# Performance work log

Measured on AMD Instinct MI355X. Metric: run time of the kernel, lower is better.

The kernel has to match this reference:

```python
import jax, jax.numpy as jnp
import numpy as np

B, S, H = 1, 2048, 1024
NH, KVH, HD = 16, 4, 64
E, TOPK, F = 8, 2, 2048
EPS = 1e-5
THETA = 10000.0


def setup_inputs() -> dict:
    key = jax.random.key(0)
    ks = jax.random.split(key, 12)
    s = 0.02
    return {
        "hidden_states": jax.random.normal(ks[0], (B, S, H), jnp.float32),
        "position_ids": jnp.arange(S, dtype=jnp.int64).reshape(1, S),
        "ln1_w": jnp.ones((H,), jnp.float32),
        "ln2_w": jnp.ones((H,), jnp.float32),
        "wq": jax.random.normal(ks[1], (NH * HD, H), jnp.float32) * s,
        "wk": jax.random.normal(ks[2], (KVH * HD, H), jnp.float32) * s,
        "wv": jax.random.normal(ks[3], (KVH * HD, H), jnp.float32) * s,
        "wo": jax.random.normal(ks[4], (H, NH * HD), jnp.float32) * s,
        "gate_w": jax.random.normal(ks[5], (E, H), jnp.float32) * s,
        "w1": jax.random.normal(ks[6], (E, F, H), jnp.float32) * s,
        "w2": jax.random.normal(ks[7], (E, H, F), jnp.float32) * s,
        "w3": jax.random.normal(ks[8], (E, F, H), jnp.float32) * s,
    }


def rmsnorm(x, w, eps=EPS):
    xf = x.astype(jnp.float32)
    v = jnp.mean(xf * xf, axis=-1, keepdims=True)
    return (xf * jax.lax.rsqrt(v + eps)).astype(x.dtype) * w


def rotate_half(x):
    x1, x2 = jnp.split(x, 2, axis=-1)
    return jnp.concatenate([-x2, x1], axis=-1)


def attention(x, position_ids, wq, wk, wv, wo):
    q = (x @ wq.T).reshape(B, S, NH, HD).transpose(0, 2, 1, 3)   # [B,NH,S,HD]
    k = (x @ wk.T).reshape(B, S, KVH, HD).transpose(0, 2, 1, 3)  # [B,KVH,S,HD]
    v = (x @ wv.T).reshape(B, S, KVH, HD).transpose(0, 2, 1, 3)
    inv_freq = 1.0 / (THETA ** (jnp.arange(0, HD, 2, dtype=jnp.float32) / HD))
    ang = position_ids.astype(jnp.float32)[:, :, None] * inv_freq  # [B,S,HD/2]
    emb = jnp.concatenate([ang, ang], axis=-1)                     # [B,S,HD]
    cos = jnp.cos(emb)[:, None]                                    # [B,1,S,HD]
    sin = jnp.sin(emb)[:, None]
    q = q * cos + rotate_half(q) * sin
    k = k * cos + rotate_half(k) * sin
    rep = NH // KVH
    k = jnp.repeat(k, rep, axis=1)
    v = jnp.repeat(v, rep, axis=1)
    scores = jnp.einsum("bhqd,bhkd->bhqk", q, k) / np.sqrt(HD).astype(np.float32)
    causal = jnp.tril(jnp.ones((S, S), bool))
    scores = jnp.where(causal, scores, jnp.finfo(scores.dtype).min)
    attn = jax.nn.softmax(scores, axis=-1)
    ctx = jnp.einsum("bhqk,bhkd->bhqd", attn, v)
    ctx = ctx.transpose(0, 2, 1, 3).reshape(B, S, NH * HD)
    return ctx @ wo.T


def moe(x, gate_w, w1, w2, w3):
    xt = x.reshape(-1, H)                                  # [T,H]
    router_logits = xt @ gate_w.T                          # [T,E]
    probs = jax.nn.softmax(router_logits.astype(jnp.float32), axis=-1)
    topw, topi = jax.lax.top_k(probs, TOPK)                # [T,K]
    topw = topw / jnp.sum(topw, axis=-1, keepdims=True)
    topw = topw.astype(x.dtype)
    # combine weights per expert: [T,E]
    cw = jnp.sum(topw[..., None] * jax.nn.one_hot(topi, E, dtype=x.dtype), axis=1)
    h1 = jnp.einsum("th,efh->etf", xt, w1)
    h3 = jnp.einsum("th,efh->etf", xt, w3)
    g = jax.nn.silu(h1) * h3                               # [E,T,F]
    y = jnp.einsum("etf,ehf->eth", g, w2)                  # [E,T,H]
    out = jnp.einsum("eth,te->th", y, cw)
    return out.reshape(B, S, H), router_logits


def reference(hidden_states, position_ids, ln1_w, ln2_w, wq, wk, wv, wo,
              gate_w, w1, w2, w3):
    residual = hidden_states
    h = rmsnorm(hidden_states, ln1_w)
    h = attention(h, position_ids, wq, wk, wv, wo)
    h = residual + h
    residual = h
    h = rmsnorm(h, ln2_w)
    h, router_logits = moe(h, gate_w, w1, w2, w3)
    h = residual + h
    return h, router_logits
```

## Files before the change

### kernel.cpp

```cpp
#include <hip/hip_runtime.h>
#include <hip/hip_bf16.h>
#include <cstdint>

typedef unsigned short u16;
typedef __attribute__((ext_vector_type(8))) short bh8;
typedef __attribute__((ext_vector_type(4))) short sh4;
typedef __attribute__((ext_vector_type(4))) float fx4;

#define NTOK 2048
#define HDIM 1024
#define NE 8
#define FDIM 2048

#define VMCNT(n) asm volatile("s_waitcnt vmcnt(" #n ")" ::: "memory")
#define LGKM0()  asm volatile("s_waitcnt lgkmcnt(0)" ::: "memory")
#define SBAR()   __builtin_amdgcn_s_barrier()
#define SCB()    __builtin_amdgcn_sched_barrier(0)

__device__ __forceinline__ u16 f2bf(float f) {
    __hip_bfloat16 h = __float2bfloat16(f);
    return __builtin_bit_cast(u16, h);
}

__device__ __forceinline__ void gll16(const void* g, void* l) {
    __builtin_amdgcn_global_load_lds(
        (const __attribute__((address_space(1))) void*)g,
        (__attribute__((address_space(3))) void*)l, 16, 0, 0);
}

#define N8_WQ 131072
#define N8_WK 32768
#define N8_WV 32768
#define N8_WO 131072
#define N8_W  2097152
#define B0q 0
#define B1k (B0q + N8_WQ)
#define B2v (B1k + N8_WK)
#define B3o (B2v + N8_WV)
#define B4a (B3o + N8_WO)
#define B5b (B4a + N8_W)
#define B6c (B5b + N8_W)
#define N8TOT (B6c + N8_W)

__global__ __launch_bounds__(256)
void convert_all_k(const float* __restrict__ wq, const float* __restrict__ wk,
                   const float* __restrict__ wv, const float* __restrict__ wo,
                   const float* __restrict__ w1, const float* __restrict__ w2,
                   const float* __restrict__ w3, u16* __restrict__ arena) {
    int i = blockIdx.x * 256 + threadIdx.x;
    const int stride = gridDim.x * 256;
    for (; i < N8TOT; i += stride) {
        const float* src;
        int base;
        if (i < B1k)      { src = wq; base = B0q; }
        else if (i < B2v) { src = wk; base = B1k; }
        else if (i < B3o) { src = wv; base = B2v; }
        else if (i < B4a) { src = wo; base = B3o; }
        else if (i < B5b) { src = w1; base = B4a; }
        else if (i < B6c) { src = w2; base = B5b; }
        else              { src = w3; base = B6c; }
        const size_t li = (size_t)(i - base) * 8;
        const fx4 a = *(const fx4*)&src[li];
        const fx4 b = *(const fx4*)&src[li + 4];
        bh8 o;
        #pragma unroll
        for (int j = 0; j < 4; ++j) {
            o[j]     = (short)f2bf(a[j]);
            o[j + 4] = (short)f2bf(b[j]);
        }
        *(bh8*)&arena[(size_t)i * 8] = o;
    }
}

__global__ __launch_bounds__(256)
void rope_table_k(float* __restrict__ cosT, float* __restrict__ sinT) {
    int idx = blockIdx.x * 256 + threadIdx.x;
    int t = idx >> 5, i = idx & 31;
    float freq = powf(10000.0f, -(float)i * (1.0f / 32.0f));
    float ang = (float)t * freq;
    float s, c;
    sincosf(ang, &s, &c);
    cosT[idx] = c;
    sinT[idx] = s;
}

__global__ __launch_bounds__(256)
void rmsnorm_k(const float* __restrict__ X, const float* __restrict__ W, u16* __restrict__ O) {
    const int t = blockIdx.x;
    const int tid = threadIdx.x;
    const fx4 v = *(const fx4*)&X[(size_t)t * HDIM + tid * 4];
    float ss = v[0]*v[0] + v[1]*v[1] + v[2]*v[2] + v[3]*v[3];
    #pragma unroll
    for (int o = 1; o < 64; o <<= 1) ss += __shfl_xor(ss, o);
    __shared__ float red[4];
    if ((tid & 63) == 0) red[tid >> 6] = ss;
    __syncthreads();
    const float inv = rsqrtf((red[0] + red[1] + red[2] + red[3]) * (1.0f / HDIM) + 1e-5f);
    const fx4 w = *(const fx4*)&W[tid * 4];
    sh4 o4;
    #pragma unroll
    for (int i = 0; i < 4; ++i) o4[i] = (short)f2bf(v[i] * inv * w[i]);
    *(sh4*)&O[(size_t)t * HDIM + tid * 4] = o4;
}

__global__ __launch_bounds__(256)
void rmsnorm2_router_k(const float* __restrict__ X, const float* __restrict__ W,
                       const float* __restrict__ GW, u16* __restrict__ O,
                       float* __restrict__ LOGI) {
    const int t = blockIdx.x;
    const int tid = threadIdx.x;
    const fx4 v = *(const fx4*)&X[(size_t)t * HDIM + tid * 4];
    float ss = v[0]*v[0] + v[1]*v[1] + v[2]*v[2] + v[3]*v[3];
    #pragma unroll
    for (int o = 1; o < 64; o <<= 1) ss += __shfl_xor(ss, o);
    __shared__ float red[4];
    if ((tid & 63) == 0) red[tid >> 6] = ss;
    __syncthreads();
    const float inv = rsqrtf((red[0] + red[1] + red[2] + red[3]) * (1.0f / HDIM) + 1e-5f);
    const fx4 w = *(const fx4*)&W[tid * 4];
    fx4 xn;
    #pragma unroll
    for (int i = 0; i < 4; ++i) xn[i] = v[i] * inv * w[i];
    sh4 o4;
    #pragma unroll
    for (int i = 0; i < 4; ++i) o4[i] = (short)f2bf(xn[i]);
    *(sh4*)&O[(size_t)t * HDIM + tid * 4] = o4;

    float part[NE];
    #pragma unroll
    for (int e = 0; e < NE; ++e) {
        const fx4 g = *(const fx4*)&GW[(size_t)e * HDIM + tid * 4];
        part[e] = g[0]*xn[0] + g[1]*xn[1] + g[2]*xn[2] + g[3]*xn[3];
    }
    #pragma unroll
    for (int e = 0; e < NE; ++e)
        #pragma unroll
        for (int o = 1; o < 64; o <<= 1) part[e] += __shfl_xor(part[e], o);
    __shared__ float red8[4][NE];
    if ((tid & 63) == 0) {
        #pragma unroll
        for (int e = 0; e < NE; ++e) red8[tid >> 6][e] = part[e];
    }
    __syncthreads();
    if (tid < NE)
        LOGI[(size_t)t * NE + tid] = red8[0][tid] + red8[1][tid] + red8[2][tid] + red8[3][tid];
}

__global__ __launch_bounds__(256)
void router_topk_k(const float* __restrict__ LOGI, int* __restrict__ counts,
                   int* __restrict__ tokslot, float* __restrict__ wtb) {
    const int t = blockIdx.x * 256 + threadIdx.x;
    float l[NE];
    #pragma unroll
    for (int e = 0; e < NE; ++e) l[e] = LOGI[(size_t)t * NE + e];
    int i0 = 0;
    #pragma unroll
    for (int e = 1; e < NE; ++e) if (l[e] > l[i0]) i0 = e;
    int i1 = (i0 == 0) ? 1 : 0;
    #pragma unroll
    for (int e = 0; e < NE; ++e) if (e != i0 && l[e] > l[i1]) i1 = e;
    float e1 = __expf(l[i1] - l[i0]);
    float w0 = 1.0f / (1.0f + e1);
    float w1 = 1.0f - w0;
    int p0 = atomicAdd(&counts[i0], 1);
    tokslot[i0 * NTOK + p0] = t * 2;
    wtb[i0 * NTOK + p0] = w0;
    int p1 = atomicAdd(&counts[i1], 1);
    tokslot[i1 * NTOK + p1] = t * 2 + 1;
    wtb[i1 * NTOK + p1] = w1;
}

template<int EPI>
__global__ __launch_bounds__(256)
void gemm_bt(const u16* __restrict__ A, const u16* __restrict__ B,
             u16* __restrict__ Cb, float* __restrict__ Cf,
             const int N, const int K,
             const float* __restrict__ aux0, const float* __restrict__ aux1) {
    __shared__ u16 As[2][64 * 32];
    __shared__ u16 Bs[2][64 * 32];

    const int tid = threadIdx.x;
    const int lane = tid & 63;
    const int wid = tid >> 6;
    const int lrow = lane & 15, lgrp = lane >> 4;
    const int wm = wid * 16;
    const int soff = (lgrp ^ ((lrow >> 1) & 3)) * 8;

    const int m0 = blockIdx.y * 64;
    const int n0 = blockIdx.x * 64;

    const int gseg = ((tid & 3) ^ ((tid >> 3) & 3)) * 8;
    const u16* apg = A + (size_t)(m0 + (tid >> 2)) * K + gseg;
    const u16* bpg = B + (size_t)(n0 + (tid >> 2)) * K + gseg;

    fx4 acc[4];
    #pragma unroll
    for (int i = 0; i < 4; ++i) acc[i] = fx4{0.f, 0.f, 0.f, 0.f};

    gll16(apg, &As[0][wid * 512]);
    gll16(bpg, &Bs[0][wid * 512]);

    for (int k0 = 0; k0 < K; k0 += 64) {
        gll16(apg + k0 + 32, &As[1][wid * 512]);
        gll16(bpg + k0 + 32, &Bs[1][wid * 512]);
        VMCNT(2); SBAR(); SCB();
        {
            const bh8 af = *(const bh8*)&As[0][(wm + lrow) * 32 + soff];
            #pragma unroll
            for (int ni = 0; ni < 4; ++ni) {
                const bh8 bf = *(const bh8*)&Bs[0][(ni * 16 + lrow) * 32 + soff];
                acc[ni] = __builtin_amdgcn_mfma_f32_16x16x32_bf16(af, bf, acc[ni], 0, 0, 0);
            }
        }
        LGKM0(); SBAR();
        {
            const int kn = (k0 + 64 < K) ? k0 + 64 : k0;
            gll16(apg + kn, &As[0][wid * 512]);
            gll16(bpg + kn, &Bs[0][wid * 512]);
        }
        VMCNT(2); SBAR(); SCB();
        {
            const bh8 af = *(const bh8*)&As[1][(wm + lrow) * 32 + soff];
            #pragma unroll
            for (int ni = 0; ni < 4; ++ni) {
                const bh8 bf = *(const bh8*)&Bs[1][(ni * 16 + lrow) * 32 + soff];
                acc[ni] = __builtin_amdgcn_mfma_f32_16x16x32_bf16(af, bf, acc[ni], 0, 0, 0);
            }
        }
        LGKM0(); SBAR();
    }
    VMCNT(0);

    #pragma unroll
    for (int j = 0; j < 4; ++j) {
        const int r = m0 + wm + lgrp * 4 + j;
        if (EPI == 3) {
            #pragma unroll
            for (int ni = 0; ni < 2; ++ni) {
                const int d = ni * 16 + lrow;
                const float cv = aux0[r * 32 + d];
                const float sv = aux1[r * 32 + d];
                const float v0 = acc[ni][j];
                const float v1 = acc[ni + 2][j];
                Cb[(size_t)r * N + n0 + d]      = f2bf(v0 * cv - v1 * sv);
                Cb[(size_t)r * N + n0 + d + 32] = f2bf(v1 * cv + v0 * sv);
            }
        } else {
            #pragma unroll
            for (int ni = 0; ni < 4; ++ni) {
                const int c = n0 + ni * 16 + lrow;
                const float v = acc[ni][j];
                if (EPI == 1) Cf[(size_t)r * N + c] = v + aux0[(size_t)r * N + c];
                if (EPI == 2) Cb[(size_t)r * N + c] = f2bf(v);
            }
        }
    }
}

__global__ __launch_bounds__(256)
void transpose_v_k(const u16* __restrict__ V, u16* __restrict__ VT) {
    __shared__ u16 Ls[64 * 66];
    const int tid = threadIdx.x;
    const int c0 = blockIdx.x * 64;
    const int t0 = blockIdx.y * 64;

    const int r = tid >> 2;
    const int seg = (tid & 3) * 16;
    const size_t src = (size_t)(t0 + r) * 256 + c0 + seg;
    *(bh8*)&Ls[r * 66 + seg]     = *(const bh8*)&V[src];
    *(bh8*)&Ls[r * 66 + seg + 8] = *(const bh8*)&V[src + 8];
    __syncthreads();
    const int c = tid >> 2;
    bh8 o0, o1;
    #pragma unroll
    for (int j = 0; j < 8; ++j) {
        o0[j] = (short)Ls[(seg + j) * 66 + c];
        o1[j] = (short)Ls[(seg + 8 + j) * 66 + c];
    }
    const size_t dst = (size_t)(c0 + c) * NTOK + t0 + seg;
    *(bh8*)&VT[dst]     = o0;
    *(bh8*)&VT[dst + 8] = o1;
}

__global__ __launch_bounds__(256)
void attn_part_k(const u16* __restrict__ Q, const u16* __restrict__ Kg,
                 const u16* __restrict__ VTg, float* __restrict__ pacc,
                 float* __restrict__ pl) {
    const int qt = blockIdx.x;
    const int h = blockIdx.y;
    const int c = blockIdx.z;
    if (c * 8 > qt) return;
    const int t0 = c * 8;
    const int tend = min(qt + 1, t0 + 8);
    const int kvh = h >> 2;

    const int tid = threadIdx.x;
    const int lane = tid & 63;
    const int wid = tid >> 6;
    const int lrow = lane & 15, lgrp = lane >> 4;

    __shared__ u16 Ks[64 * 66];
    __shared__ u16 Vs[64 * 66];
    __shared__ u16 Ps[4][16 * 66];

    const int qbase = qt * 64 + wid * 16;

    bh8 qf[2];
    #pragma unroll
    for (int kf = 0; kf < 2; ++kf)
        qf[kf] = *(const bh8*)&Q[(size_t)(qbase + lrow) * 1024 + h * 64 + kf * 32 + lgrp * 8];

    fx4 acc[4];
    #pragma unroll
    for (int ni = 0; ni < 4; ++ni) acc[ni] = fx4{0.f, 0.f, 0.f, 0.f};
    float lsum[4];
    #pragma unroll
    for (int j = 0; j < 4; ++j) lsum[j] = 0.f;

    const int srow = tid >> 2;
    const int sseg = (tid & 3) * 16;

    size_t gk = (size_t)(t0 * 64 + srow) * 256 + kvh * 64 + sseg;
    size_t gv = (size_t)(kvh * 64 + srow) * NTOK + t0 * 64 + sseg;
    bh8 kva = *(const bh8*)&Kg[gk];
    bh8 kvb = *(const bh8*)&Kg[gk + 8];
    bh8 vva = *(const bh8*)&VTg[gv];
    bh8 vvb = *(const bh8*)&VTg[gv + 8];

    for (int it = t0; it < tend; ++it) {
        const int kv0 = it * 64;
        __syncthreads();
        *(bh8*)&Ks[srow * 66 + sseg]     = kva;
        *(bh8*)&Ks[srow * 66 + sseg + 8] = kvb;
        *(bh8*)&Vs[srow * 66 + sseg]     = vva;
        *(bh8*)&Vs[srow * 66 + sseg + 8] = vvb;
        __syncthreads();

        const int itn = (it + 1 < tend) ? it + 1 : it;
        const size_t gk2 = (size_t)(itn * 64 + srow) * 256 + kvh * 64 + sseg;
        const size_t gv2 = (size_t)(kvh * 64 + srow) * NTOK + itn * 64 + sseg;
        kva = *(const bh8*)&Kg[gk2];
        kvb = *(const bh8*)&Kg[gk2 + 8];
        vva = *(const bh8*)&VTg[gv2];
        vvb = *(const bh8*)&VTg[gv2 + 8];

        fx4 s[4];
        #pragma unroll
        for (int nf = 0; nf < 4; ++nf) s[nf] = fx4{0.f, 0.f, 0.f, 0.f};
        #pragma unroll
        for (int kf = 0; kf < 2; ++kf) {
            #pragma unroll
            for (int nf = 0; nf < 4; ++nf) {
                const bh8 kfr = *(const bh8*)&Ks[(nf * 16 + lrow) * 66 + kf * 32 + lgrp * 8];
                s[nf] = __builtin_amdgcn_mfma_f32_16x16x32_bf16(qf[kf], kfr, s[nf], 0, 0, 0);
            }
        }

        #pragma unroll
        for (int nf = 0; nf < 4; ++nf)
            #pragma unroll
            for (int j = 0; j < 4; ++j) {
                const int qr = qbase + lgrp * 4 + j;
                const int kp = kv0 + nf * 16 + lrow;
                float p = __expf(fmaf(s[nf][j], 0.125f, -24.0f));
                p = (kp > qr) ? 0.f : p;
                s[nf][j] = p;
                lsum[j] += p;
            }

        u16* pw = Ps[wid];
        #pragma unroll
        for (int nf = 0; nf < 4; ++nf)
            #pragma unroll
            for (int j = 0; j < 4; ++j)
                pw[(lgrp * 4 + j) * 66 + nf * 16 + lrow] = f2bf(s[nf][j]);

        #pragma unroll
        for (int kf = 0; kf < 2; ++kf) {
            const bh8 pa = *(const bh8*)&pw[lrow * 66 + kf * 32 + lgrp * 8];
            #pragma unroll
            for (int ni = 0; ni < 4; ++ni) {
                const bh8 vb = *(const bh8*)&Vs[(ni * 16 + lrow) * 66 + kf * 32 + lgrp * 8];
                acc[ni] = __builtin_amdgcn_mfma_f32_16x16x32_bf16(pa, vb, acc[ni], 0, 0, 0);
            }
        }
    }

    #pragma unroll
    for (int j = 0; j < 4; ++j) {
        float l = lsum[j];
        #pragma unroll
        for (int o = 1; o < 16; o <<= 1) l += __shfl_xor(l, o);
        lsum[j] = l;
    }

    #pragma unroll
    for (int j = 0; j < 4; ++j) {
        const int r = qbase + lgrp * 4 + j;
        const size_t base = ((size_t)(h * NTOK + r) * 4 + c) * 64;
        #pragma unroll
        for (int ni = 0; ni < 4; ++ni)
            pacc[base + ni * 16 + lrow] = acc[ni][j];
        if (lrow == 0)
            pl[(size_t)(h * NTOK + r) * 4 + c] = lsum[j];
    }
}

__global__ __launch_bounds__(256)
void attn_combine_k(const float* __restrict__ pacc, const float* __restrict__ pl,
                    u16* __restrict__ O) {
    const int idx = blockIdx.x * 4 + (threadIdx.x >> 6);
    const int d = threadIdx.x & 63;
    const int h = idx >> 11;
    const int qrow = idx & 2047;
    const int nch = (qrow >> 9) + 1;

    float den = 0.f, num = 0.f;
    for (int c = 0; c < nch; ++c) {
        den += pl[(size_t)idx * 4 + c];
        num += pacc[((size_t)idx * 4 + c) * 64 + d];
    }
    O[(size_t)qrow * 1024 + h * 64 + d] = f2bf(num / den);
}

__global__ __launch_bounds__(256)
void moe_up_k(const u16* __restrict__ X, const u16* __restrict__ W1b,
              const u16* __restrict__ W3b, const int* __restrict__ counts,
              const int* __restrict__ tokslot, u16* __restrict__ G) {
    const int e = blockIdx.z;
    const int cnt = counts[e];
    const int m0 = blockIdx.y * 64;
    if (m0 >= cnt) return;
    const int n0 = blockIdx.x * 128;

    __shared__ u16 As[2][64 * 32];
    __shared__ u16 B1s[2][128 * 32];
    __shared__ u16 B3s[2][128 * 32];

    const int tid = threadIdx.x;
    const int lane = tid & 63, wid = tid >> 6;
    const int wm = (wid >> 1) * 32, wn = (wid & 1) * 64;
    const int lrow = lane & 15, lgrp = lane >> 4;
    const int soff = (lgrp ^ ((lrow >> 1) & 3)) * 8;

    const int gseg = ((tid & 3) ^ ((tid >> 3) & 3)) * 8;
    const int arow = m0 + (tid >> 2);
    const int tok = (arow < cnt) ? (tokslot[e * NTOK + arow] >> 1) : 0;
    const u16* apg = X + (size_t)tok * HDIM + gseg;
    const size_t eoff = (size_t)e * FDIM * HDIM;
    const u16* b1pg = W1b + eoff + (size_t)(n0 + (tid >> 2)) * HDIM + gseg;
    const u16* b3pg = W3b + eoff + (size_t)(n0 + (tid >> 2)) * HDIM + gseg;
    const size_t rr = (size_t)64 * HDIM;

    fx4 acc1[2][4], acc3[2][4];
    #pragma unroll
    for (int i = 0; i < 2; ++i)
        #pragma unroll
        for (int j = 0; j < 4; ++j) {
            acc1[i][j] = fx4{0.f, 0.f, 0.f, 0.f};
            acc3[i][j] = fx4{0.f, 0.f, 0.f, 0.f};
        }

    gll16(apg, &As[0][wid * 512]);
    gll16(b1pg, &B1s[0][wid * 512]);
    gll16(b1pg + rr, &B1s[0][2048 + wid * 512]);
    gll16(b3pg, &B3s[0][wid * 512]);
    gll16(b3pg + rr, &B3s[0][2048 + wid * 512]);

#define MOE_UP_COMPUTE(BUF)                                                          \
    {                                                                                \
        bh8 af[2], b1f[4], b3f[4];                                                   \
        _Pragma("unroll")                                                            \
        for (int mi = 0; mi < 2; ++mi)                                               \
            af[mi] = *(const bh8*)&As[BUF][(wm + mi * 16 + lrow) * 32 + soff];       \
        _Pragma("unroll")                                                            \
        for (int ni = 0; ni < 4; ++ni) {                                             \
            b1f[ni] = *(const bh8*)&B1s[BUF][(wn + ni * 16 + lrow) * 32 + soff];     \
            b3f[ni] = *(const bh8*)&B3s[BUF][(wn + ni * 16 + lrow) * 32 + soff];     \
        }                                                                            \
        _Pragma("unroll")                                                            \
        for (int mi = 0; mi < 2; ++mi)                                               \
            _Pragma("unroll")                                                        \
            for (int ni = 0; ni < 4; ++ni) {                                         \
                acc1[mi][ni] = __builtin_amdgcn_mfma_f32_16x16x32_bf16(af[mi], b1f[ni], acc1[mi][ni], 0, 0, 0); \
                acc3[mi][ni] = __builtin_amdgcn_mfma_f32_16x16x32_bf16(af[mi], b3f[ni], acc3[mi][ni], 0, 0, 0); \
            }                                                                        \
    }

    for (int k0 = 0; k0 < HDIM; k0 += 64) {
        {
            const int kn = k0 + 32;
            gll16(apg + kn, &As[1][wid * 512]);
            gll16(b1pg + kn, &B1s[1][wid * 512]);
            gll16(b1pg + rr + kn, &B1s[1][2048 + wid * 512]);
            gll16(b3pg + kn, &B3s[1][wid * 512]);
            gll16(b3pg + rr + kn, &B3s[1][2048 + wid * 512]);
        }
        VMCNT(5); SBAR(); SCB();
        MOE_UP_COMPUTE(0)
        LGKM0(); SBAR();
        {
            const int kn = (k0 + 64 < HDIM) ? k0 + 64 : k0;
            gll16(apg + kn, &As[0][wid * 512]);
            gll16(b1pg + kn, &B1s[0][wid * 512]);
            gll16(b1pg + rr + kn, &B1s[0][2048 + wid * 512]);
            gll16(b3pg + kn, &B3s[0][wid * 512]);
            gll16(b3pg + rr + kn, &B3s[0][2048 + wid * 512]);
        }
        VMCNT(5); SBAR(); SCB();
        MOE_UP_COMPUTE(1)
        LGKM0(); SBAR();
    }
    VMCNT(0);
#undef MOE_UP_COMPUTE

    #pragma unroll
    for (int mi = 0; mi < 2; ++mi)
        #pragma unroll
        for (int j = 0; j < 4; ++j) {
            const int r = m0 + wm + mi * 16 + lgrp * 4 + j;
            if (r < cnt) {
                #pragma unroll
                for (int ni = 0; ni < 4; ++ni) {
                    const int c = n0 + wn + ni * 16 + lrow;
                    const float h1 = acc1[mi][ni][j];
                    const float h3 = acc3[mi][ni][j];
                    const float gv = h1 / (1.0f + __expf(-h1)) * h3;
                    G[((size_t)e * NTOK + r) * FDIM + c] = f2bf(gv);
                }
            }
        }
}

__global__ __launch_bounds__(256)
void moe_down_k(const u16* __restrict__ G, const u16* __restrict__ W2b,
                const int* __restrict__ counts, const int* __restrict__ tokslot,
                const float* __restrict__ wtb, float* __restrict__ MO) {
    const int e = blockIdx.z;
    const int cnt = counts[e];
    const int m0 = blockIdx.y * 64;
    if (m0 >= cnt) return;
    const int n0 = blockIdx.x * 64;

    __shared__ u16 As[2][64 * 32];
    __shared__ u16 Bs[2][64 * 32];

    const int tid = threadIdx.x;
    const int lane = tid & 63, wid = tid >> 6;
    const int wm = wid * 16;
    const int lrow = lane & 15, lgrp = lane >> 4;
    const int soff = (lgrp ^ ((lrow >> 1) & 3)) * 8;

    const int gseg = ((tid & 3) ^ ((tid >> 3) & 3)) * 8;
    const u16* apg = G + ((size_t)e * NTOK + m0 + (tid >> 2)) * FDIM + gseg;
    const u16* bpg = W2b + (size_t)e * HDIM * FDIM + (size_t)(n0 + (tid >> 2)) * FDIM + gseg;

    fx4 acc[4];
    #pragma unroll
    for (int i = 0; i < 4; ++i) acc[i] = fx4{0.f, 0.f, 0.f, 0.f};

    gll16(apg, &As[0][wid * 512]);
    gll16(bpg, &Bs[0][wid * 512]);

    for (int k0 = 0; k0 < FDIM; k0 += 64) {
        gll16(apg + k0 + 32, &As[1][wid * 512]);
        gll16(bpg + k0 + 32, &Bs[1][wid * 512]);
        VMCNT(2); SBAR(); SCB();
        {
            const bh8 af = *(const bh8*)&As[0][(wm + lrow) * 32 + soff];
            #pragma unroll
            for (int ni = 0; ni < 4; ++ni) {
                const bh8 bf = *(const bh8*)&Bs[0][(ni * 16 + lrow) * 32 + soff];
                acc[ni] = __builtin_amdgcn_mfma_f32_16x16x32_bf16(af, bf, acc[ni], 0, 0, 0);
            }
        }
        LGKM0(); SBAR();
        {
            const int kn = (k0 + 64 < FDIM) ? k0 + 64 : k0;
            gll16(apg + kn, &As[0][wid * 512]);
            gll16(bpg + kn, &Bs[0][wid * 512]);
        }
        VMCNT(2); SBAR(); SCB();
        {
            const bh8 af = *(const bh8*)&As[1][(wm + lrow) * 32 + soff];
            #pragma unroll
            for (int ni = 0; ni < 4; ++ni) {
                const bh8 bf = *(const bh8*)&Bs[1][(ni * 16 + lrow) * 32 + soff];
                acc[ni] = __builtin_amdgcn_mfma_f32_16x16x32_bf16(af, bf, acc[ni], 0, 0, 0);
            }
        }
        LGKM0(); SBAR();
    }
    VMCNT(0);

    #pragma unroll
    for (int j = 0; j < 4; ++j) {
        const int r = m0 + wm + lgrp * 4 + j;
        if (r < cnt) {
            const int ts = tokslot[e * NTOK + r];
            const float wgt = wtb[e * NTOK + r];
            const int tt = ts >> 1;
            const int sl = ts & 1;
            #pragma unroll
            for (int ni = 0; ni < 4; ++ni) {
                const int c = n0 + ni * 16 + lrow;
                MO[((size_t)sl * NTOK + tt) * HDIM + c] = acc[ni][j] * wgt;
            }
        }
    }
}

__global__ __launch_bounds__(256)
void final_add_k(const float* __restrict__ A, const float* __restrict__ B0,
                 const float* __restrict__ B1, float* __restrict__ O) {
    const size_t i = ((size_t)blockIdx.x * 256 + threadIdx.x) * 4;
    const fx4 a = *(const fx4*)&A[i];
    const fx4 b = *(const fx4*)&B0[i];
    const fx4 c = *(const fx4*)&B1[i];
    fx4 r;
    #pragma unroll
    for (int k = 0; k < 4; ++k) r[k] = a[k] + b[k] + c[k];
    *(fx4*)&O[i] = r;
}

extern "C" void kernel_launch(void* const* d_in, const int* in_sizes, int n_in,
                              void* d_out, int out_size, void* d_ws, size_t ws_size,
                              hipStream_t stream) {
    const float* x   = (const float*)d_in[0];
    const float* ln1 = (const float*)d_in[2];
    const float* ln2 = (const float*)d_in[3];
    const float* wq  = (const float*)d_in[4];
    const float* wk  = (const float*)d_in[5];
    const float* wv  = (const float*)d_in[6];
    const float* wo  = (const float*)d_in[7];
    const float* gw  = (const float*)d_in[8];
    const float* w1  = (const float*)d_in[9];
    const float* w2  = (const float*)d_in[10];
    const float* w3  = (const float*)d_in[11];

    float* out_h = (float*)d_out;
    float* out_logits = out_h + (size_t)NTOK * HDIM;

    uint8_t* wsb = (uint8_t*)d_ws;
    size_t off = 0;
    auto alloc = [&](size_t bytes) -> void* {
        void* ptr = wsb + off;
        off = (off + bytes + 255) & ~(size_t)255;
        return ptr;
    };
    u16*   xn1    = (u16*)alloc((size_t)NTOK * HDIM * 2);
    u16*   qb     = (u16*)alloc((size_t)NTOK * 1024 * 2);
    u16*   kb     = (u16*)alloc((size_t)NTOK * 256 * 2);
    u16*   vb     = (u16*)alloc((size_t)NTOK * 256 * 2);
    u16*   vbt    = (u16*)alloc((size_t)256 * NTOK * 2);
    u16*   ctxb   = (u16*)alloc((size_t)NTOK * 1024 * 2);
    float* hattn  = (float*)alloc((size_t)NTOK * HDIM * 4);
    u16*   xn2    = (u16*)alloc((size_t)NTOK * HDIM * 2);
    float* cosT   = (float*)alloc((size_t)NTOK * 32 * 4);
    float* sinT   = (float*)alloc((size_t)NTOK * 32 * 4);
    int*   counts = (int*)alloc(NE * 4);
    int*   tokslot= (int*)alloc((size_t)NE * NTOK * 4);
    float* wtb    = (float*)alloc((size_t)NE * NTOK * 4);
    u16*   gbuf   = (u16*)alloc((size_t)NE * NTOK * FDIM * 2);
    float* moeb   = (float*)alloc((size_t)2 * NTOK * HDIM * 4);
    u16*   arena  = (u16*)alloc((size_t)N8TOT * 8 * 2);
    u16*   wqb    = arena;
    u16*   wkb    = arena + (size_t)B1k * 8;
    u16*   wvb    = arena + (size_t)B2v * 8;
    u16*   wob    = arena + (size_t)B3o * 8;
    u16*   w1b    = arena + (size_t)B4a * 8;
    u16*   w2b    = arena + (size_t)B5b * 8;
    u16*   w3b    = arena + (size_t)B6c * 8;

    float* pacc = (float*)gbuf;
    float* pl   = pacc + (size_t)16 * NTOK * 4 * 64;

    hipMemsetAsync(counts, 0, NE * 4, stream);

    convert_all_k<<<2048, 256, 0, stream>>>(wq, wk, wv, wo, w1, w2, w3, arena);

    rope_table_k<<<256, 256, 0, stream>>>(cosT, sinT);
    rmsnorm_k<<<NTOK, 256, 0, stream>>>(x, ln1, xn1);
    gemm_bt<3><<<dim3(16, 32), 256, 0, stream>>>(xn1, wqb, qb, nullptr, 1024, HDIM, cosT, sinT);
    gemm_bt<3><<<dim3(4, 32), 256, 0, stream>>>(xn1, wkb, kb, nullptr, 256, HDIM, cosT, sinT);
    gemm_bt<2><<<dim3(4, 32), 256, 0, stream>>>(xn1, wvb, vb, nullptr, 256, HDIM, nullptr, nullptr);
    transpose_v_k<<<dim3(4, 32), 256, 0, stream>>>(vb, vbt);
    attn_part_k<<<dim3(32, 16, 4), 256, 0, stream>>>(qb, kb, vbt, pacc, pl);
    attn_combine_k<<<8192, 256, 0, stream>>>(pacc, pl, ctxb);
    gemm_bt<1><<<dim3(16, 32), 256, 0, stream>>>(ctxb, wob, nullptr, hattn, 1024, 1024, x, nullptr);
    rmsnorm2_router_k<<<NTOK, 256, 0, stream>>>(hattn, ln2, gw, xn2, out_logits);
    router_topk_k<<<8, 256, 0, stream>>>(out_logits, counts, tokslot, wtb);
    moe_up_k<<<dim3(16, 32, NE), 256, 0, stream>>>(xn2, w1b, w3b, counts, tokslot, gbuf);
    moe_down_k<<<dim3(16, 32, NE), 256, 0, stream>>>(gbuf, w2b, counts, tokslot, wtb, moeb);
    final_add_k<<<NTOK, 256, 0, stream>>>(hattn, moeb, moeb + (size_t)NTOK * HDIM, out_h);
}
```

Measured before the change: 387.5 us.

## Quad-buffer GEMM k-loop and interleave w1/w3 rows for smaller MoE up tiles

All GEMM kernels move from a double-buffered to a four-stage LDS pipeline, keeping three k-slices in flight (vmcnt 6) to hide global-load latency. The weight conversion kernel now interleaves w1 and w3 rows in groups of 16 into one combined matrix. This lets moe_up_k use the same simple 64x64 tile kernel, with the paired accumulators giving h1 and h3 for the SiLU-gate epilogue. The trade is more LDS per block and 4x as many MoE up blocks, each with less reuse of the A tile.

```diff
diff --git a/kernel.cpp b/kernel.cpp
--- a/kernel.cpp
+++ b/kernel.cpp
@@ -38,9 +38,8 @@
 #define B2v (B1k + N8_WK)
 #define B3o (B2v + N8_WV)
 #define B4a (B3o + N8_WO)
-#define B5b (B4a + N8_W)
-#define B6c (B5b + N8_W)
-#define N8TOT (B6c + N8_W)
+#define B5w (B4a + 2 * N8_W)
+#define N8TOT (B5w + N8_W)
 
 __global__ __launch_bounds__(256)
 void convert_all_k(const float* __restrict__ wq, const float* __restrict__ wk,
@@ -51,15 +50,22 @@
     const int stride = gridDim.x * 256;
     for (; i < N8TOT; i += stride) {
         const float* src;
-        int base;
-        if (i < B1k)      { src = wq; base = B0q; }
-        else if (i < B2v) { src = wk; base = B1k; }
-        else if (i < B3o) { src = wv; base = B2v; }
-        else if (i < B4a) { src = wo; base = B3o; }
-        else if (i < B5b) { src = w1; base = B4a; }
-        else if (i < B6c) { src = w2; base = B5b; }
-        else              { src = w3; base = B6c; }
-        const size_t li = (size_t)(i - base) * 8;
+        size_t li;
+        if (i < B1k)      { src = wq; li = (size_t)(i - B0q) * 8; }
+        else if (i < B2v) { src = wk; li = (size_t)(i - B1k) * 8; }
+        else if (i < B3o) { src = wv; li = (size_t)(i - B2v) * 8; }
+        else if (i < B4a) { src = wo; li = (size_t)(i - B3o) * 8; }
+        else if (i < B5w) {
+            const int idx8 = i - B4a;
+            const int Rg = idx8 >> 7;
+            const int col8 = idx8 & 127;
+            const int e = Rg >> 12;
+            const int R = Rg & 4095;
+            const int fb = R >> 5, part = (R >> 4) & 1, fr = R & 15;
+            const int f = fb * 16 + fr;
+            src = part ? w3 : w1;
+            li = ((size_t)e * 2048 + f) * 1024 + (size_t)col8 * 8;
+        } else            { src = w2; li = (size_t)(i - B5w) * 8; }
         const fx4 a = *(const fx4*)&src[li];
         const fx4 b = *(const fx4*)&src[li + 4];
         bh8 o;
@@ -176,8 +182,8 @@
              u16* __restrict__ Cb, float* __restrict__ Cf,
              const int N, const int K,
              const float* __restrict__ aux0, const float* __restrict__ aux1) {
-    __shared__ u16 As[2][64 * 32];
-    __shared__ u16 Bs[2][64 * 32];
+    __shared__ u16 As[4][64 * 32];
+    __shared__ u16 Bs[4][64 * 32];
 
     const int tid = threadIdx.x;
     const int lane = tid & 63;
@@ -197,39 +203,34 @@
     #pragma unroll
     for (int i = 0; i < 4; ++i) acc[i] = fx4{0.f, 0.f, 0.f, 0.f};
 
-    gll16(apg, &As[0][wid * 512]);
-    gll16(bpg, &Bs[0][wid * 512]);
-
-    for (int k0 = 0; k0 < K; k0 += 64) {
-        gll16(apg + k0 + 32, &As[1][wid * 512]);
-        gll16(bpg + k0 + 32, &Bs[1][wid * 512]);
-        VMCNT(2); SBAR(); SCB();
-        {
-            const bh8 af = *(const bh8*)&As[0][(wm + lrow) * 32 + soff];
-            #pragma unroll
-            for (int ni = 0; ni < 4; ++ni) {
-                const bh8 bf = *(const bh8*)&Bs[0][(ni * 16 + lrow) * 32 + soff];
-                acc[ni] = __builtin_amdgcn_mfma_f32_16x16x32_bf16(af, bf, acc[ni], 0, 0, 0);
-            }
-        }
-        LGKM0(); SBAR();
-        {
-            const int kn = (k0 + 64 < K) ? k0 + 64 : k0;
-            gll16(apg + kn, &As[0][wid * 512]);
-            gll16(bpg + kn, &Bs[0][wid * 512]);
-        }
-        VMCNT(2); SBAR(); SCB();
-        {
-            const bh8 af = *(const bh8*)&As[1][(wm + lrow) * 32 + soff];
-            #pragma unroll
-            for (int ni = 0; ni < 4; ++ni) {
-                const bh8 bf = *(const bh8*)&Bs[1][(ni * 16 + lrow) * 32 + soff];
-                acc[ni] = __builtin_amdgcn_mfma_f32_16x16x32_bf16(af, bf, acc[ni], 0, 0, 0);
-            }
-        }
-        LGKM0(); SBAR();
+#define G_STG(BUF, KK) gll16(apg + (KK), &As[BUF][wid * 512]); \
+                       gll16(bpg + (KK), &Bs[BUF][wid * 512]);
+#define G_CMP(BUF)                                                             \
+    {                                                                          \
+        const bh8 af = *(const bh8*)&As[BUF][(wm + lrow) * 32 + soff];         \
+        _Pragma("unroll")                                                      \
+        for (int ni = 0; ni < 4; ++ni) {                                       \
+            const bh8 bf = *(const bh8*)&Bs[BUF][(ni * 16 + lrow) * 32 + soff];\
+            acc[ni] = __builtin_amdgcn_mfma_f32_16x16x32_bf16(af, bf, acc[ni], 0, 0, 0); \
+        }                                                                      \
+    }
+#define G_PHASE(BUF_ST, KOFF, BUF_CM)                                          \
+    { const int kn = (k0 + (KOFF) < K) ? k0 + (KOFF) : 0; G_STG(BUF_ST, kn) }  \
+    VMCNT(6); SBAR(); SCB();                                                   \
+    G_CMP(BUF_CM)                                                              \
+    LGKM0(); SBAR();
+
+    G_STG(0, 0) G_STG(1, 32) G_STG(2, 64)
+    for (int k0 = 0; k0 < K; k0 += 128) {
+        G_PHASE(3, 96, 0)
+        G_PHASE(0, 128, 1)
+        G_PHASE(1, 160, 2)
+        G_PHASE(2, 192, 3)
     }
     VMCNT(0);
+#undef G_STG
+#undef G_CMP
+#undef G_PHASE
 
     #pragma unroll
     for (int j = 0; j < 4; ++j) {
@@ -424,112 +425,79 @@
 }
 
 __global__ __launch_bounds__(256)
-void moe_up_k(const u16* __restrict__ X, const u16* __restrict__ W1b,
-              const u16* __restrict__ W3b, const int* __restrict__ counts,
-              const int* __restrict__ tokslot, u16* __restrict__ G) {
+void moe_up_k(const u16* __restrict__ X, const u16* __restrict__ W13,
+              const int* __restrict__ counts, const int* __restrict__ tokslot,
+              u16* __restrict__ G) {
     const int e = blockIdx.z;
     const int cnt = counts[e];
     const int m0 = blockIdx.y * 64;
     if (m0 >= cnt) return;
-    const int n0 = blockIdx.x * 128;
-
-    __shared__ u16 As[2][64 * 32];
-    __shared__ u16 B1s[2][128 * 32];
-    __shared__ u16 B3s[2][128 * 32];
+    const int n0 = blockIdx.x * 64;
+
+    __shared__ u16 As[4][64 * 32];
+    __shared__ u16 Bs[4][64 * 32];
 
     const int tid = threadIdx.x;
-    const int lane = tid & 63, wid = tid >> 6;
-    const int wm = (wid >> 1) * 32, wn = (wid & 1) * 64;
+    const int lane = tid & 63;
+    const int wid = tid >> 6;
     const int lrow = lane & 15, lgrp = lane >> 4;
+    const int wm = wid * 16;
     const int soff = (lgrp ^ ((lrow >> 1) & 3)) * 8;
 
     const int gseg = ((tid & 3) ^ ((tid >> 3) & 3)) * 8;
     const int arow = m0 + (tid >> 2);
     const int tok = (arow < cnt) ? (tokslot[e * NTOK + arow] >> 1) : 0;
     const u16* apg = X + (size_t)tok * HDIM + gseg;
-    const size_t eoff = (size_t)e * FDIM * HDIM;
-    const u16* b1pg = W1b + eoff + (size_t)(n0 + (tid >> 2)) * HDIM + gseg;
-    const u16* b3pg = W3b + eoff + (size_t)(n0 + (tid >> 2)) * HDIM + gseg;
-    const size_t rr = (size_t)64 * HDIM;
-
-    fx4 acc1[2][4], acc3[2][4];
-    #pragma unroll
-    for (int i = 0; i < 2; ++i)
-        #pragma unroll
-        for (int j = 0; j < 4; ++j) {
-            acc1[i][j] = fx4{0.f, 0.f, 0.f, 0.f};
-            acc3[i][j] = fx4{0.f, 0.f, 0.f, 0.f};
-        }
-
-    gll16(apg, &As[0][wid * 512]);
-    gll16(b1pg, &B1s[0][wid * 512]);
-    gll16(b1pg + rr, &B1s[0][2048 + wid * 512]);
-    gll16(b3pg, &B3s[0][wid * 512]);
-    gll16(b3pg + rr, &B3s[0][2048 + wid * 512]);
-
-#define MOE_UP_COMPUTE(BUF)                                                          \
-    {                                                                                \
-        bh8 af[2], b1f[4], b3f[4];                                                   \
-        _Pragma("unroll")                                                            \
-        for (int mi = 0; mi < 2; ++mi)                                               \
-            af[mi] = *(const bh8*)&As[BUF][(wm + mi * 16 + lrow) * 32 + soff];       \
-        _Pragma("unroll")                                                            \
-        for (int ni = 0; ni < 4; ++ni) {                                             \
-            b1f[ni] = *(const bh8*)&B1s[BUF][(wn + ni * 16 + lrow) * 32 + soff];     \
-            b3f[ni] = *(const bh8*)&B3s[BUF][(wn + ni * 16 + lrow) * 32 + soff];     \
-        }                                                                            \
-        _Pragma("unroll")                                                            \
-        for (int mi = 0; mi < 2; ++mi)                                               \
-            _Pragma("unroll")                                                        \
-            for (int ni = 0; ni < 4; ++ni) {                                         \
-                acc1[mi][ni] = __builtin_amdgcn_mfma_f32_16x16x32_bf16(af[mi], b1f[ni], acc1[mi][ni], 0, 0, 0); \
-                acc3[mi][ni] = __builtin_amdgcn_mfma_f32_16x16x32_bf16(af[mi], b3f[ni], acc3[mi][ni], 0, 0, 0); \
-            }                                                                        \
-    }
-
-    for (int k0 = 0; k0 < HDIM; k0 += 64) {
-        {
-            const int kn = k0 + 32;
-            gll16(apg + kn, &As[1][wid * 512]);
-            gll16(b1pg + kn, &B1s[1][wid * 512]);
-            gll16(b1pg + rr + kn, &B1s[1][2048 + wid * 512]);
-            gll16(b3pg + kn, &B3s[1][wid * 512]);
-            gll16(b3pg + rr + kn, &B3s[1][2048 + wid * 512]);
-        }
-        VMCNT(5); SBAR(); SCB();
-        MOE_UP_COMPUTE(0)
-        LGKM0(); SBAR();
-        {
-            const int kn = (k0 + 64 < HDIM) ? k0 + 64 : k0;
-            gll16(apg + kn, &As[0][wid * 512]);
-            gll16(b1pg + kn, &B1s[0][wid * 512]);
-            gll16(b1pg + rr + kn, &B1s[0][2048 + wid * 512]);
-            gll16(b3pg + kn, &B3s[0][wid * 512]);
-            gll16(b3pg + rr + kn, &B3s[0][2048 + wid * 512]);
-        }
-        VMCNT(5); SBAR(); SCB();
-        MOE_UP_COMPUTE(1)
-        LGKM0(); SBAR();
+    const u16* bpg = W13 + (size_t)(e * 4096 + n0 + (tid >> 2)) * HDIM + gseg;
+
+    fx4 acc[4];
+    #pragma unroll
+    for (int i = 0; i < 4; ++i) acc[i] = fx4{0.f, 0.f, 0.f, 0.f};
+
+#define U_STG(BUF, KK) gll16(apg + (KK), &As[BUF][wid * 512]); \
+                       gll16(bpg + (KK), &Bs[BUF][wid * 512]);
+#define U_CMP(BUF)                                                             \
+    {                                                                          \
+        const bh8 af = *(const bh8*)&As[BUF][(wm + lrow) * 32 + soff];         \
+        _Pragma("unroll")                                                      \
+        for (int ni = 0; ni < 4; ++ni) {                                       \
+            const bh8 bf = *(const bh8*)&Bs[BUF][(ni * 16 + lrow) * 32 + soff];\
+            acc[ni] = __builtin_amdgcn_mfma_f32_16x16x32_bf16(af, bf, acc[ni], 0, 0, 0); \
+        }                                                                      \
+    }
+#define U_PHASE(BUF_ST, KOFF, BUF_CM)                                          \
+    { const int kn = (k0 + (KOFF) < HDIM) ? k0 + (KOFF) : 0; U_STG(BUF_ST, kn) } \
+    VMCNT(6); SBAR(); SCB();                                                   \
+    U_CMP(BUF_CM)                                                              \
+    LGKM0(); SBAR();
+
+    U_STG(0, 0) U_STG(1, 32) U_STG(2, 64)
+    for (int k0 = 0; k0 < HDIM; k0 += 128) {
+        U_PHASE(3, 96, 0)
+        U_PHASE(0, 128, 1)
+        U_PHASE(1, 160, 2)
+        U_PHASE(2, 192, 3)
     }
     VMCNT(0);
-#undef MOE_UP_COMPUTE
-
-    #pragma unroll
-    for (int mi = 0; mi < 2; ++mi)
-        #pragma unroll
-        for (int j = 0; j < 4; ++j) {
-            const int r = m0 + wm + mi * 16 + lgrp * 4 + j;
-            if (r < cnt) {
-                #pragma unroll
-                for (int ni = 0; ni < 4; ++ni) {
-                    const int c = n0 + wn + ni * 16 + lrow;
-                    const float h1 = acc1[mi][ni][j];
-                    const float h3 = acc3[mi][ni][j];
-                    const float gv = h1 / (1.0f + __expf(-h1)) * h3;
-                    G[((size_t)e * NTOK + r) * FDIM + c] = f2bf(gv);
-                }
+#undef U_STG
+#undef U_CMP
+#undef U_PHASE
+
+    #pragma unroll
+    for (int j = 0; j < 4; ++j) {
+        const int r = m0 + wm + lgrp * 4 + j;
+        if (r < cnt) {
+            #pragma unroll
+            for (int pi = 0; pi < 2; ++pi) {
+                const int ni = pi * 2;
+                const int gcol = ((n0 + ni * 16) >> 5) * 16 + lrow;
+                const float h1 = acc[ni][j];
+                const float h3 = acc[ni + 1][j];
+                const float gv = h1 / (1.0f + __expf(-h1)) * h3;
+                G[((size_t)e * NTOK + r) * FDIM + gcol] = f2bf(gv);
             }
         }
+    }
 }
 
 __global__ __launch_bounds__(256)
@@ -542,13 +510,14 @@
     if (m0 >= cnt) return;
     const int n0 = blockIdx.x * 64;
 
-    __shared__ u16 As[2][64 * 32];
-    __shared__ u16 Bs[2][64 * 32];
+    __shared__ u16 As[4][64 * 32];
+    __shared__ u16 Bs[4][64 * 32];
 
     const int tid = threadIdx.x;
-    const int lane = tid & 63, wid = tid >> 6;
+    const int lane = tid & 63;
+    const int wid = tid >> 6;
+    const int lrow = lane & 15, lgrp = lane >> 4;
     const int wm = wid * 16;
-    const int lrow = lane & 15, lgrp = lane >> 4;
     const int soff = (lgrp ^ ((lrow >> 1) & 3)) * 8;
 
     const int gseg = ((tid & 3) ^ ((tid >> 3) & 3)) * 8;
@@ -559,39 +528,34 @@
     #pragma unroll
     for (int i = 0; i < 4; ++i) acc[i] = fx4{0.f, 0.f, 0.f, 0.f};
 
-    gll16(apg, &As[0][wid * 512]);
-    gll16(bpg, &Bs[0][wid * 512]);
-
-    for (int k0 = 0; k0 < FDIM; k0 += 64) {
-        gll16(apg + k0 + 32, &As[1][wid * 512]);
-        gll16(bpg + k0 + 32, &Bs[1][wid * 512]);
-        VMCNT(2); SBAR(); SCB();
-        {
-            const bh8 af = *(const bh8*)&As[0][(wm + lrow) * 32 + soff];
-            #pragma unroll
-            for (int ni = 0; ni < 4; ++ni) {
-                const bh8 bf = *(const bh8*)&Bs[0][(ni * 16 + lrow) * 32 + soff];
-                acc[ni] = __builtin_amdgcn_mfma_f32_16x16x32_bf16(af, bf, acc[ni], 0, 0, 0);
-            }
-        }
-        LGKM0(); SBAR();
-        {
-            const int kn = (k0 + 64 < FDIM) ? k0 + 64 : k0;
-            gll16(apg + kn, &As[0][wid * 512]);
-            gll16(bpg + kn, &Bs[0][wid * 512]);
-        }
-        VMCNT(2); SBAR(); SCB();
-        {
-            const bh8 af = *(const bh8*)&As[1][(wm + lrow) * 32 + soff];
-            #pragma unroll
-            for (int ni = 0; ni < 4; ++ni) {
-                const bh8 bf = *(const bh8*)&Bs[1][(ni * 16 + lrow) * 32 + soff];
-                acc[ni] = __builtin_amdgcn_mfma_f32_16x16x32_bf16(af, bf, acc[ni], 0, 0, 0);
-            }
-        }
-        LGKM0(); SBAR();
+#define D_STG(BUF, KK) gll16(apg + (KK), &As[BUF][wid * 512]); \
+                       gll16(bpg + (KK), &Bs[BUF][wid * 512]);
+#define D_CMP(BUF)                                                             \
+    {                                                                          \
+        const bh8 af = *(const bh8*)&As[BUF][(wm + lrow) * 32 + soff];         \
+        _Pragma("unroll")                                                      \
+        for (int ni = 0; ni < 4; ++ni) {                                       \
+            const bh8 bf = *(const bh8*)&Bs[BUF][(ni * 16 + lrow) * 32 + soff];\
+            acc[ni] = __builtin_amdgcn_mfma_f32_16x16x32_bf16(af, bf, acc[ni], 0, 0, 0); \
+        }                                                                      \
+    }
+#define D_PHASE(BUF_ST, KOFF, BUF_CM)                                          \
+    { const int kn = (k0 + (KOFF) < FDIM) ? k0 + (KOFF) : 0; D_STG(BUF_ST, kn) } \
+    VMCNT(6); SBAR(); SCB();                                                   \
+    D_CMP(BUF_CM)                                                              \
+    LGKM0(); SBAR();
+
+    D_STG(0, 0) D_STG(1, 32) D_STG(2, 64)
+    for (int k0 = 0; k0 < FDIM; k0 += 128) {
+        D_PHASE(3, 96, 0)
+        D_PHASE(0, 128, 1)
+        D_PHASE(1, 160, 2)
+        D_PHASE(2, 192, 3)
     }
     VMCNT(0);
+#undef D_STG
+#undef D_CMP
+#undef D_PHASE
 
     #pragma unroll
     for (int j = 0; j < 4; ++j) {
@@ -668,9 +632,8 @@
     u16*   wkb    = arena + (size_t)B1k * 8;
     u16*   wvb    = arena + (size_t)B2v * 8;
     u16*   wob    = arena + (size_t)B3o * 8;
-    u16*   w1b    = arena + (size_t)B4a * 8;
-    u16*   w2b    = arena + (size_t)B5b * 8;
-    u16*   w3b    = arena + (size_t)B6c * 8;
+    u16*   w13b   = arena + (size_t)B4a * 8;
+    u16*   w2b    = arena + (size_t)B5w * 8;
 
     float* pacc = (float*)gbuf;
     float* pl   = pacc + (size_t)16 * NTOK * 4 * 64;
@@ -690,7 +653,7 @@
     gemm_bt<1><<<dim3(16, 32), 256, 0, stream>>>(ctxb, wob, nullptr, hattn, 1024, 1024, x, nullptr);
     rmsnorm2_router_k<<<NTOK, 256, 0, stream>>>(hattn, ln2, gw, xn2, out_logits);
     router_topk_k<<<8, 256, 0, stream>>>(out_logits, counts, tokslot, wtb);
-    moe_up_k<<<dim3(16, 32, NE), 256, 0, stream>>>(xn2, w1b, w3b, counts, tokslot, gbuf);
+    moe_up_k<<<dim3(64, 32, NE), 256, 0, stream>>>(xn2, w13b, counts, tokslot, gbuf);
     moe_down_k<<<dim3(16, 32, NE), 256, 0, stream>>>(gbuf, w2b, counts, tokslot, wtb, moeb);
     final_add_k<<<NTOK, 256, 0, stream>>>(hattn, moeb, moeb + (size_t)NTOK * HDIM, out_h);
 }
```

Result: no change. 389.8 us (+0.6%).
